# Kernel optimization log

Hardware: AMD Instinct MI355X
Metric: run time of the kernel (lower is better)

Reference implementation:

```python
import jax, jax.numpy as jnp
import numpy as np

EPS = 1e-5

def _layer_norm(x, g, b):
    mu = jnp.mean(x, axis=-1, keepdims=True)
    var = jnp.mean(jnp.square(x - mu), axis=-1, keepdims=True)
    return (x - mu) * jax.lax.rsqrt(var + EPS) * g + b

def setup_inputs() -> dict:
    key = jax.random.key(0)
    Bsz, N, H = 2, 384, 128
    ks = jax.random.split(key, 16)
    s = 1.0 / np.sqrt(H)
    d = {
        'h_nodes': jax.random.normal(ks[0], (Bsz, N, H), jnp.float32),
        'h_edges': jax.random.normal(ks[1], (Bsz, N, N, H), jnp.float32),
        'adj_matrix_mask': (jax.random.uniform(ks[2], (Bsz, N, N)) < 0.5).astype(jnp.float32),
    }
    for i, nm in enumerate(['U', 'V', 'A', 'B', 'C']):
        d[nm + '_w'] = jax.random.normal(ks[3 + 2 * i], (H, H), jnp.float32) * s
        d[nm + '_b'] = jax.random.normal(ks[4 + 2 * i], (H,), jnp.float32) * s
    d['gh'] = jnp.ones((H,), jnp.float32); d['bh'] = jnp.zeros((H,), jnp.float32)
    d['ge'] = jnp.ones((H,), jnp.float32); d['be'] = jnp.zeros((H,), jnp.float32)
    return d

def reference(h_nodes, h_edges, adj_matrix_mask, U_w, U_b, V_w, V_b, A_w, A_b, B_w, B_b, C_w, C_b, gh, bh, ge, be):
    # torch Linear: y = x @ W^T + b
    Uh = h_nodes @ U_w.T + U_b            # [B,N,H]
    Vh = h_nodes @ V_w.T + V_b            # [B,N,H] (j features)
    Ah = h_nodes @ A_w.T + A_b
    Bh = h_nodes @ B_w.T + B_b
    Ce = h_edges @ C_w.T + C_b            # [B,N,N,H]
    e_upd = Ah[:, :, None, :] + Bh[:, None, :, :] + Ce   # [B,N,N,H]
    gates = jax.nn.sigmoid(e_upd)
    msgs = gates * Vh[:, None, :, :] * adj_matrix_mask[..., None]
    agg = jnp.sum(msgs, axis=2)           # sum over j -> [B,N,H]
    h_upd = jax.nn.relu(_layer_norm(Uh + agg, gh, bh))
    e_act = jax.nn.relu(_layer_norm(e_upd, ge, be))
    return (h_nodes + h_upd, h_edges + e_act)
```

## Files before the change

kernel.cpp:

```cpp
#include <hip/hip_runtime.h>
#include <hip/hip_bf16.h>

typedef __bf16 bf16_t;
typedef __bf16 bf16x8 __attribute__((ext_vector_type(8)));
typedef __bf16 bf16x4 __attribute__((ext_vector_type(4)));
typedef float f32x4 __attribute__((ext_vector_type(4)));

#define HD 128
#define NN 384
#define ROWS 768
#define SZ 98304
#define JC 3
#define CWPITCH 272

__device__ inline int detect_f32(const void* p) {
    const unsigned short* u = (const unsigned short*)p;
    int bad = 0;
    #pragma unroll
    for (int k = 0; k < 128; ++k) {
        int e = (u[k] >> 7) & 0xFF;
        bad += (e < 110 || e > 135) ? 1 : 0;
    }
    return bad >= 16 ? 1 : 0;
}

__global__ __launch_bounds__(64) void detect_kernel(const void* p, float* ws) {
    if (threadIdx.x == 0)
        *(int*)((char*)ws + (size_t)7 * SZ * 4) = detect_f32(p);
}

__device__ inline int read_flag(const float* ws) {
    return *(const int*)((const char*)ws + (size_t)7 * SZ * 4);
}

template<int CTRL>
__device__ __attribute__((always_inline)) inline float dpp_add(float x) {
    int xi = __builtin_bit_cast(int, x);
    int yi = __builtin_amdgcn_update_dpp(0, xi, CTRL, 0xF, 0xF, true);
    return x + __builtin_bit_cast(float, yi);
}
__device__ __attribute__((always_inline)) inline float row16_sum(float x) {
    x = dpp_add<0xB1>(x);
    x = dpp_add<0x4E>(x);
    x = dpp_add<0x124>(x);
    x = dpp_add<0x128>(x);
    return x;
}

__device__ __attribute__((always_inline)) inline void ld8(const float* p, float* o) {
    f32x4 a = *(const f32x4*)p;
    f32x4 b = *(const f32x4*)(p + 4);
    o[0] = a[0]; o[1] = a[1]; o[2] = a[2]; o[3] = a[3];
    o[4] = b[0]; o[5] = b[1]; o[6] = b[2]; o[7] = b[3];
}
__device__ __attribute__((always_inline)) inline void ld8(const bf16_t* p, float* o) {
    bf16x8 v = *(const bf16x8*)p;
    #pragma unroll
    for (int e = 0; e < 8; ++e) o[e] = (float)v[e];
}
__device__ __attribute__((always_inline)) inline bf16x8 ld8b(const float* p) {
    f32x4 a = *(const f32x4*)p;
    f32x4 b = *(const f32x4*)(p + 4);
    bf16x8 v;
    #pragma unroll
    for (int e = 0; e < 4; ++e) { v[e] = (bf16_t)a[e]; v[e + 4] = (bf16_t)b[e]; }
    return v;
}
__device__ __attribute__((always_inline)) inline bf16x8 ld8b(const bf16_t* p) { return *(const bf16x8*)p; }
__device__ __attribute__((always_inline)) inline bf16x4 ld4b(const float* p) {
    f32x4 a = *(const f32x4*)p;
    bf16x4 v;
    #pragma unroll
    for (int e = 0; e < 4; ++e) v[e] = (bf16_t)a[e];
    return v;
}
__device__ __attribute__((always_inline)) inline bf16x4 ld4b(const bf16_t* p) { return *(const bf16x4*)p; }

template<typename T>
__device__ void node_body(float* x,
    const T* h_nodes, const T* Uw, const T* Ub, const T* Vw, const T* Vb,
    const T* Aw, const T* Ab, const T* Bw, const T* Bb, const T* Cb,
    float* ws)
{
    const int row = blockIdx.x, m = blockIdx.y, t = threadIdx.x;
    x[t] = (float)h_nodes[row * HD + t];
    __syncthreads();

    const T* Ws[4] = {Aw, Bw, Vw, Uw};
    float bias;
    if (m == 0)      bias = (float)Ab[t] + (float)Cb[t];
    else if (m == 1) bias = (float)Bb[t];
    else if (m == 2) bias = (float)Vb[t];
    else             bias = (float)Ub[t];

    float acc = bias;
    const T* W = Ws[m] + (size_t)t * HD;
    #pragma unroll
    for (int kk = 0; kk < 16; ++kk) {
        float w8[8];
        ld8(W + kk * 8, w8);
        #pragma unroll
        for (int e = 0; e < 8; ++e) acc = fmaf(x[kk * 8 + e], w8[e], acc);
    }
    if (m == 1 || m == 2)
        ((bf16_t*)(ws + (size_t)m * SZ))[row * HD + t] = (bf16_t)acc;
    else
        ws[(size_t)m * SZ + row * HD + t] = acc;
}

__global__ __launch_bounds__(128) void node_linear(
    const void* h_nodes, const void* Uw, const void* Ub, const void* Vw, const void* Vb,
    const void* Aw, const void* Ab, const void* Bw, const void* Bb, const void* Cb,
    float* __restrict__ ws)
{
    __shared__ __align__(16) float x[HD];
    if (read_flag(ws))
        node_body<float>(x, (const float*)h_nodes, (const float*)Uw, (const float*)Ub,
                         (const float*)Vw, (const float*)Vb, (const float*)Aw, (const float*)Ab,
                         (const float*)Bw, (const float*)Bb, (const float*)Cb, ws);
    else
        node_body<bf16_t>(x, (const bf16_t*)h_nodes, (const bf16_t*)Uw, (const bf16_t*)Ub,
                          (const bf16_t*)Vw, (const bf16_t*)Vb, (const bf16_t*)Aw, (const bf16_t*)Ab,
                          (const bf16_t*)Bw, (const bf16_t*)Bb, (const bf16_t*)Cb, ws);
}

struct Smem {
    bf16_t sCw[128 * (CWPITCH / 2)];
    float sAhC[HD], sGe[HD], sBe[HD];
    float sAgg[8][HD];
};

template<typename T>
__device__ void edge_body(Smem& sm,
    const T* __restrict__ h_edges, const T* __restrict__ adj,
    const T* __restrict__ Cw, const T* __restrict__ ge, const T* __restrict__ be,
    const float* __restrict__ ws, float* __restrict__ wagg, float* __restrict__ out)
{
    const int i = blockIdx.x, jc = blockIdx.y, b = blockIdx.z;
    const int bi = b * NN + i;
    const int t = threadIdx.x;
    const int l = t & 63, w = t >> 6;
    const int lr = l & 15, lg = l >> 4;
    const int hbase = lg * 4;

    {
        const int slot = t & 15;
        #pragma unroll
        for (int p = 0; p < 4; ++p) {
            const int row = p * 32 + (t >> 4);
            bf16x8 v = ld8b(&Cw[(size_t)row * HD + slot * 8]);
            *(bf16x8*)((char*)sm.sCw + row * CWPITCH + slot * 16) = v;
        }
    }
    if (t < HD) {
        sm.sAhC[t] = ws[0 * SZ + bi * HD + t];
        sm.sGe[t]  = (float)ge[t];
        sm.sBe[t]  = (float)be[t];
    }

    __syncthreads();

    const T* Ebase = h_edges + (size_t)bi * NN * HD;
    const int j = jc * 128 + w * 16 + lr;
    const T* Erow = &Ebase[(size_t)j * HD];

    const float mk = (float)adj[(size_t)bi * NN + j];
    bf16x4 res[8];
    #pragma unroll
    for (int ct = 0; ct < 8; ++ct)
        res[ct] = ld4b(&Erow[ct * 16 + hbase]);

    const bf16_t* Bhrow = (const bf16_t*)(ws + 1 * SZ) + ((size_t)b * NN + j) * HD;
    const bf16_t* Vhrow = (const bf16_t*)(ws + 2 * SZ) + ((size_t)b * NN + j) * HD;
    bf16x4 bhv[8], vhv[8];
    #pragma unroll
    for (int ct = 0; ct < 8; ++ct) {
        bhv[ct] = *(const bf16x4*)&Bhrow[ct * 16 + hbase];
        vhv[ct] = *(const bf16x4*)&Vhrow[ct * 16 + hbase];
    }

    f32x4 acc[8];
    #pragma unroll
    for (int ct = 0; ct < 8; ++ct) acc[ct] = (f32x4){0.f, 0.f, 0.f, 0.f};
    #pragma unroll
    for (int ks = 0; ks < 4; ++ks) {
        bf16x8 a = ld8b(&Erow[ks * 32 + lg * 8]);
        #pragma unroll
        for (int ct = 0; ct < 8; ++ct) {
            bf16x8 Bf = *(const bf16x8*)((const char*)sm.sCw +
                          (ct * 16 + lr) * CWPITCH + (((ks << 2) | lg)) * 16);
            acc[ct] = __builtin_amdgcn_mfma_f32_16x16x32_bf16(Bf, a, acc[ct], 0, 0, 0);
        }
    }

    float* Orow = out + SZ + ((size_t)bi * NN + j) * HD;

    float sum = 0.f, ssq = 0.f;
    #pragma unroll
    for (int ct = 0; ct < 8; ++ct) {
        f32x4 e = acc[ct];
        f32x4 av = *(const f32x4*)&sm.sAhC[ct * 16 + hbase];
        #pragma unroll
        for (int r = 0; r < 4; ++r) e[r] = e[r] + av[r] + (float)bhv[ct][r];
        acc[ct] = e;
        #pragma unroll
        for (int r = 0; r < 4; ++r) { sum += e[r]; ssq = fmaf(e[r], e[r], ssq); }
    }
    sum += __shfl_xor(sum, 16); ssq += __shfl_xor(ssq, 16);
    sum += __shfl_xor(sum, 32); ssq += __shfl_xor(ssq, 32);
    const float mean = sum * (1.f / HD);
    const float rstd = rsqrtf(ssq * (1.f / HD) - mean * mean + 1e-5f);

    f32x4 agg4[8];
    #pragma unroll
    for (int ct = 0; ct < 8; ++ct) {
        f32x4 ge4 = *(const f32x4*)&sm.sGe[ct * 16 + hbase];
        f32x4 be4 = *(const f32x4*)&sm.sBe[ct * 16 + hbase];
        f32x4 o;
        #pragma unroll
        for (int r = 0; r < 4; ++r) {
            const float ee = acc[ct][r];
            const float g = __builtin_amdgcn_rcpf(1.f + exp2f(ee * -1.44269504f));
            agg4[ct][r] = g * mk * (float)vhv[ct][r];
            float a = (ee - mean) * rstd;
            a = fmaf(a, ge4[r], be4[r]);
            a = fmaxf(a, 0.f);
            o[r] = (float)res[ct][r] + a;
        }
        *(f32x4*)&Orow[ct * 16 + hbase] = o;
    }

    #pragma unroll
    for (int ct = 0; ct < 8; ++ct)
        #pragma unroll
        for (int r = 0; r < 4; ++r)
            agg4[ct][r] = row16_sum(agg4[ct][r]);
    if (lr == 0) {
        #pragma unroll
        for (int ct = 0; ct < 8; ++ct)
            *(f32x4*)&sm.sAgg[w][ct * 16 + hbase] = agg4[ct];
    }
    __syncthreads();

    if (t < HD) {
        float p = sm.sAgg[0][t] + sm.sAgg[1][t] + sm.sAgg[2][t] + sm.sAgg[3][t]
                + sm.sAgg[4][t] + sm.sAgg[5][t] + sm.sAgg[6][t] + sm.sAgg[7][t];
        wagg[((size_t)jc * ROWS + bi) * HD + t] = p;
    }
}

__global__ __launch_bounds__(512, 2) void edge_kernel(
    const void* h_edges, const void* adj, const void* Cw,
    const void* ge, const void* be,
    float* __restrict__ ws, float* __restrict__ out)
{
    __shared__ Smem sm;
    float* wagg = ws + 4 * SZ;
    if (read_flag(ws))
        edge_body<float>(sm, (const float*)h_edges, (const float*)adj, (const float*)Cw,
                         (const float*)ge, (const float*)be, ws, wagg, out);
    else
        edge_body<bf16_t>(sm, (const bf16_t*)h_edges, (const bf16_t*)adj, (const bf16_t*)Cw,
                          (const bf16_t*)ge, (const bf16_t*)be, ws, wagg, out);
}

template<typename T>
__device__ void node_upd_body(const T* h_nodes, const T* gh, const T* bh,
                              const float* ws, float* out)
{
    const int bi = blockIdx.x, t = threadIdx.x;
    float x0 = ws[3 * SZ + bi * HD + t];
    float x1 = ws[3 * SZ + bi * HD + t + 64];
    #pragma unroll
    for (int jc = 0; jc < JC; ++jc) {
        const float* p = ws + 4 * SZ + ((size_t)jc * ROWS + bi) * HD;
        x0 += p[t];
        x1 += p[t + 64];
    }
    float sum = x0 + x1;
    float ssq = x0 * x0 + x1 * x1;
    #pragma unroll
    for (int off = 1; off < 64; off <<= 1) {
        sum += __shfl_xor(sum, off);
        ssq += __shfl_xor(ssq, off);
    }
    const float mean = sum * (1.f / HD);
    const float rstd = rsqrtf(ssq * (1.f / HD) - mean * mean + 1e-5f);
    float a0 = fmaf((x0 - mean) * rstd, (float)gh[t],      (float)bh[t]);
    float a1 = fmaf((x1 - mean) * rstd, (float)gh[t + 64], (float)bh[t + 64]);
    a0 = fmaxf(a0, 0.f);
    a1 = fmaxf(a1, 0.f);
    out[bi * HD + t]      = (float)h_nodes[bi * HD + t]      + a0;
    out[bi * HD + t + 64] = (float)h_nodes[bi * HD + t + 64] + a1;
}

__global__ __launch_bounds__(64) void node_update(
    const void* h_nodes, const void* gh, const void* bh,
    const float* __restrict__ ws, float* __restrict__ out)
{
    if (read_flag(ws))
        node_upd_body<float>((const float*)h_nodes, (const float*)gh, (const float*)bh, ws, out);
    else
        node_upd_body<bf16_t>((const bf16_t*)h_nodes, (const bf16_t*)gh, (const bf16_t*)bh, ws, out);
}

extern "C" void kernel_launch(void* const* d_in, const int* in_sizes, int n_in,
                              void* d_out, int out_size, void* d_ws, size_t ws_size,
                              hipStream_t stream)
{
    float* ws = (float*)d_ws;
    float* out = (float*)d_out;

    detect_kernel<<<dim3(1), dim3(64), 0, stream>>>(d_in[0], ws);
    node_linear<<<dim3(ROWS, 4), dim3(128), 0, stream>>>(
        d_in[0], d_in[3], d_in[4], d_in[5], d_in[6], d_in[7], d_in[8],
        d_in[9], d_in[10], d_in[12], ws);
    edge_kernel<<<dim3(NN, JC, 2), dim3(512), 0, stream>>>(
        d_in[1], d_in[2], d_in[11], d_in[15], d_in[16], ws, out);
    node_update<<<dim3(ROWS), dim3(64), 0, stream>>>(
        d_in[0], d_in[13], d_in[14], ws, out);
}
```

Baseline: 139.8 us.

## Fold dtype detection into node_linear, shrink edge blocks, reorder aggregation

Drops the separate detect kernel and moves dtype detection into every node_linear block as a wave ballot over 64 halfwords, so one launch disappears. The edge kernel now uses 256-thread blocks over 64 j values each, doubling the j-chunk count, and the wagg buffer index range grows to match. The gate/aggregation reduction now runs before the layernorm output pass, which should shorten register live ranges. Each edge block reloads the full Cw tile for half as much work, adding redundant loads in exchange for more, smaller blocks.

```diff
diff --git a/kernel.cpp b/kernel.cpp
--- a/kernel.cpp
+++ b/kernel.cpp
@@ -10,27 +10,11 @@
 #define NN 384
 #define ROWS 768
 #define SZ 98304
-#define JC 3
+#define JC 6
 #define CWPITCH 272
 
-__device__ inline int detect_f32(const void* p) {
-    const unsigned short* u = (const unsigned short*)p;
-    int bad = 0;
-    #pragma unroll
-    for (int k = 0; k < 128; ++k) {
-        int e = (u[k] >> 7) & 0xFF;
-        bad += (e < 110 || e > 135) ? 1 : 0;
-    }
-    return bad >= 16 ? 1 : 0;
-}
-
-__global__ __launch_bounds__(64) void detect_kernel(const void* p, float* ws) {
-    if (threadIdx.x == 0)
-        *(int*)((char*)ws + (size_t)7 * SZ * 4) = detect_f32(p);
-}
-
 __device__ inline int read_flag(const float* ws) {
-    return *(const int*)((const char*)ws + (size_t)7 * SZ * 4);
+    return *(const int*)((const char*)ws + (size_t)10 * SZ * 4);
 }
 
 template<int CTRL>
@@ -114,7 +98,22 @@
     float* __restrict__ ws)
 {
     __shared__ __align__(16) float x[HD];
-    if (read_flag(ws))
+    __shared__ int flagS;
+    {
+        const int t = threadIdx.x;
+        if (t < 64) {
+            const unsigned short* u = (const unsigned short*)h_nodes;
+            int e = (u[t] >> 7) & 0xFF;
+            unsigned long long m = __ballot(e < 110 || e > 135);
+            if (t == 0) flagS = (__popcll(m) >= 8) ? 1 : 0;
+        }
+        __syncthreads();
+    }
+    const int isf32 = flagS;
+    if (blockIdx.x == 0 && blockIdx.y == 0 && threadIdx.x == 0)
+        *(int*)((char*)ws + (size_t)10 * SZ * 4) = isf32;
+
+    if (isf32)
         node_body<float>(x, (const float*)h_nodes, (const float*)Uw, (const float*)Ub,
                          (const float*)Vw, (const float*)Vb, (const float*)Aw, (const float*)Ab,
                          (const float*)Bw, (const float*)Bb, (const float*)Cb, ws);
@@ -127,7 +126,7 @@
 struct Smem {
     bf16_t sCw[128 * (CWPITCH / 2)];
     float sAhC[HD], sGe[HD], sBe[HD];
-    float sAgg[8][HD];
+    float sAgg[4][HD];
 };
 
 template<typename T>
@@ -146,8 +145,8 @@
     {
         const int slot = t & 15;
         #pragma unroll
-        for (int p = 0; p < 4; ++p) {
-            const int row = p * 32 + (t >> 4);
+        for (int p = 0; p < 8; ++p) {
+            const int row = p * 16 + (t >> 4);
             bf16x8 v = ld8b(&Cw[(size_t)row * HD + slot * 8]);
             *(bf16x8*)((char*)sm.sCw + row * CWPITCH + slot * 16) = v;
         }
@@ -161,7 +160,7 @@
     __syncthreads();
 
     const T* Ebase = h_edges + (size_t)bi * NN * HD;
-    const int j = jc * 128 + w * 16 + lr;
+    const int j = jc * 64 + w * 16 + lr;
     const T* Erow = &Ebase[(size_t)j * HD];
 
     const float mk = (float)adj[(size_t)bi * NN + j];
@@ -193,8 +192,6 @@
         }
     }
 
-    float* Orow = out + SZ + ((size_t)bi * NN + j) * HD;
-
     float sum = 0.f, ssq = 0.f;
     #pragma unroll
     for (int ct = 0; ct < 8; ++ct) {
@@ -214,42 +211,47 @@
     f32x4 agg4[8];
     #pragma unroll
     for (int ct = 0; ct < 8; ++ct) {
+        #pragma unroll
+        for (int r = 0; r < 4; ++r) {
+            const float g = __builtin_amdgcn_rcpf(1.f + exp2f(acc[ct][r] * -1.44269504f));
+            agg4[ct][r] = g * mk * (float)vhv[ct][r];
+        }
+    }
+    #pragma unroll
+    for (int ct = 0; ct < 8; ++ct)
+        #pragma unroll
+        for (int r = 0; r < 4; ++r)
+            agg4[ct][r] = row16_sum(agg4[ct][r]);
+    if (lr == 0) {
+        #pragma unroll
+        for (int ct = 0; ct < 8; ++ct)
+            *(f32x4*)&sm.sAgg[w][ct * 16 + hbase] = agg4[ct];
+    }
+    __syncthreads();
+
+    if (t < HD) {
+        float p = sm.sAgg[0][t] + sm.sAgg[1][t] + sm.sAgg[2][t] + sm.sAgg[3][t];
+        wagg[((size_t)jc * ROWS + bi) * HD + t] = p;
+    }
+
+    float* Orow = out + SZ + ((size_t)bi * NN + j) * HD;
+    #pragma unroll
+    for (int ct = 0; ct < 8; ++ct) {
         f32x4 ge4 = *(const f32x4*)&sm.sGe[ct * 16 + hbase];
         f32x4 be4 = *(const f32x4*)&sm.sBe[ct * 16 + hbase];
         f32x4 o;
         #pragma unroll
         for (int r = 0; r < 4; ++r) {
-            const float ee = acc[ct][r];
-            const float g = __builtin_amdgcn_rcpf(1.f + exp2f(ee * -1.44269504f));
-            agg4[ct][r] = g * mk * (float)vhv[ct][r];
-            float a = (ee - mean) * rstd;
+            float a = (acc[ct][r] - mean) * rstd;
             a = fmaf(a, ge4[r], be4[r]);
             a = fmaxf(a, 0.f);
             o[r] = (float)res[ct][r] + a;
         }
         *(f32x4*)&Orow[ct * 16 + hbase] = o;
     }
-
-    #pragma unroll
-    for (int ct = 0; ct < 8; ++ct)
-        #pragma unroll
-        for (int r = 0; r < 4; ++r)
-            agg4[ct][r] = row16_sum(agg4[ct][r]);
-    if (lr == 0) {
-        #pragma unroll
-        for (int ct = 0; ct < 8; ++ct)
-            *(f32x4*)&sm.sAgg[w][ct * 16 + hbase] = agg4[ct];
-    }
-    __syncthreads();
-
-    if (t < HD) {
-        float p = sm.sAgg[0][t] + sm.sAgg[1][t] + sm.sAgg[2][t] + sm.sAgg[3][t]
-                + sm.sAgg[4][t] + sm.sAgg[5][t] + sm.sAgg[6][t] + sm.sAgg[7][t];
-        wagg[((size_t)jc * ROWS + bi) * HD + t] = p;
-    }
-}
-
-__global__ __launch_bounds__(512, 2) void edge_kernel(
+}
+
+__global__ __launch_bounds__(256) void edge_kernel(
     const void* h_edges, const void* adj, const void* Cw,
     const void* ge, const void* be,
     float* __restrict__ ws, float* __restrict__ out)
@@ -311,11 +313,10 @@
     float* ws = (float*)d_ws;
     float* out = (float*)d_out;
 
-    detect_kernel<<<dim3(1), dim3(64), 0, stream>>>(d_in[0], ws);
     node_linear<<<dim3(ROWS, 4), dim3(128), 0, stream>>>(
         d_in[0], d_in[3], d_in[4], d_in[5], d_in[6], d_in[7], d_in[8],
         d_in[9], d_in[10], d_in[12], ws);
-    edge_kernel<<<dim3(NN, JC, 2), dim3(512), 0, stream>>>(
+    edge_kernel<<<dim3(NN, JC, 2), dim3(256), 0, stream>>>(
         d_in[1], d_in[2], d_in[11], d_in[15], d_in[16], ws, out);
     node_update<<<dim3(ROWS), dim3(64), 0, stream>>>(
         d_in[0], d_in[13], d_in[14], ws, out);
```

After: 144.1 us. 1.03x slower.
